# Kernel tuning notes

Measured on AMD Instinct MI355X. Metric: run time of the kernel, lower is better.

The kernel has to match this reference:

```python
import jax, jax.numpy as jnp
import numpy as np

B, D, H, E, C, TOPK = 16384, 2048, 2048, 6, 1024, 3

def setup_inputs() -> dict:
    key = jax.random.key(0)
    ks = jax.random.split(key, 8)
    s_d = 1.0 / np.sqrt(D)
    s_h = 1.0 / np.sqrt(H)
    return {
        "x": jax.random.normal(ks[0], (B, D), dtype=jnp.float32),
        "gate_W": jax.random.uniform(ks[1], (E, D), jnp.float32, -s_d, s_d),
        "gate_b": jax.random.uniform(ks[2], (E,), jnp.float32, -s_d, s_d),
        "W1": jax.random.uniform(ks[3], (E, H, D), jnp.float32, -s_d, s_d),
        "b1": jax.random.uniform(ks[4], (E, H), jnp.float32, -s_d, s_d),
        "W2": jax.random.uniform(ks[5], (E, C, H), jnp.float32, -s_h, s_h),
        "b2": jax.random.uniform(ks[6], (E, C), jnp.float32, -s_h, s_h),
    }

def reference(x, gate_W, gate_b, W1, b1, W2, b2):
    # gating: top-k sparse softmax
    gate_logits = x @ gate_W.T + gate_b                      # [B, E]
    topk_vals, topk_idx = jax.lax.top_k(gate_logits, TOPK)   # [B, K]
    neg_inf = jnp.finfo(gate_logits.dtype).min
    sparse = jnp.full_like(gate_logits, neg_inf)
    rows = jnp.arange(gate_logits.shape[0])[:, None]
    sparse = sparse.at[rows, topk_idx].set(topk_vals)
    gw = jax.nn.softmax(sparse, axis=-1)                     # [B, E]
    # dense experts: Linear -> GELU (exact, erf) -> Linear (dropout is eval no-op)
    h = jnp.einsum('bd,ehd->beh', x, W1) + b1[None]          # [B, E, H]
    h = jax.nn.gelu(h, approximate=False)
    expert_outs = jnp.einsum('beh,ech->bec', h, W2) + b2[None]  # [B, E, C]
    out = jnp.einsum('be,bec->bc', gw, expert_outs)          # masked combine
    return (out, gw)
```

## Files before the change

kernel.cpp:

```cpp
#include <hip/hip_runtime.h>
#include <hip/hip_bf16.h>
#include <math.h>

#define B_ 16384
#define D_ 2048
#define H_ 2048
#define E_ 6
#define C_ 1024

#define HALF_ (128 * 64)

typedef __attribute__((ext_vector_type(8))) short short8;
typedef __attribute__((ext_vector_type(4))) float f32x4;

__device__ __forceinline__ unsigned short f2bf(float f) {
    __hip_bfloat16 h = __float2bfloat16(f);
    return *reinterpret_cast<unsigned short*>(&h);
}

__device__ __forceinline__ void async_copy16(const unsigned short* g, unsigned short* l) {
    __builtin_amdgcn_global_load_lds(
        (const __attribute__((address_space(1))) unsigned int*)(g),
        (__attribute__((address_space(3))) unsigned int*)(l), 16, 0, 0);
}

__global__ void gate_kernel(const float* __restrict__ x, const float* __restrict__ gW,
                            const float* __restrict__ gb, float* __restrict__ gw_out,
                            int* __restrict__ counts, int* __restrict__ rowlist,
                            float* __restrict__ wtslist, unsigned short* __restrict__ xb) {
    int wave = threadIdx.x >> 6;
    int lane = threadIdx.x & 63;
    int row  = blockIdx.x * 4 + wave;
    const float* xr = x + (size_t)row * D_;
    unsigned short* xbr = xb + (size_t)row * D_;
    double acc[E_] = {0, 0, 0, 0, 0, 0};
    for (int i = 0; i < D_ / 64; ++i) {
        int d = i * 64 + lane;
        float xf = xr[d];
        xbr[d] = f2bf(xf);
        double xv = (double)xf;
#pragma unroll
        for (int e = 0; e < E_; ++e) acc[e] += xv * (double)gW[e * D_ + d];
    }
#pragma unroll
    for (int off = 32; off > 0; off >>= 1) {
#pragma unroll
        for (int e = 0; e < E_; ++e) acc[e] += __shfl_down(acc[e], off);
    }
    if (lane == 0) {
        double lg[E_];
#pragma unroll
        for (int e = 0; e < E_; ++e) lg[e] = acc[e] + (double)gb[e];
        bool used[E_] = {false, false, false, false, false, false};
        int idx[3]; double val[3];
        for (int k = 0; k < 3; ++k) {
            int best = -1; double bv = -1e300;
            for (int e = 0; e < E_; ++e)
                if (!used[e] && lg[e] > bv) { bv = lg[e]; best = e; }
            used[best] = true; idx[k] = best; val[k] = bv;
        }
        double m = val[0];
        double w[3]; double s = 0.0;
        for (int k = 0; k < 3; ++k) { w[k] = exp(val[k] - m); s += w[k]; }
        float gwv[E_] = {0.f, 0.f, 0.f, 0.f, 0.f, 0.f};
        for (int k = 0; k < 3; ++k) gwv[idx[k]] = (float)(w[k] / s);
#pragma unroll
        for (int e = 0; e < E_; ++e) gw_out[(size_t)row * E_ + e] = gwv[e];
        for (int k = 0; k < 3; ++k) {
            int e = idx[k];
            int pos = atomicAdd(&counts[e], 1);
            rowlist[(size_t)e * B_ + pos] = row * 3 + k;
            wtslist[(size_t)e * B_ + pos] = (float)(w[k] / s);
        }
    }
}

__global__ void cast_f32_bf16(const float* __restrict__ in, unsigned short* __restrict__ out, int n4) {
    int i = blockIdx.x * blockDim.x + threadIdx.x;
    if (i < n4) {
        float4 v = ((const float4*)in)[i];
        ushort4 u;
        u.x = f2bf(v.x); u.y = f2bf(v.y); u.z = f2bf(v.z); u.w = f2bf(v.w);
        ((ushort4*)out)[i] = u;
    }
}


#define PHASE_IN()                                                               \
    __builtin_amdgcn_sched_barrier(0);                                           \
    __builtin_amdgcn_s_barrier();                                                \
    asm volatile("s_waitcnt lgkmcnt(0)" ::: "memory");                           \
    __builtin_amdgcn_sched_barrier(0);                                           \
    __builtin_amdgcn_s_setprio(1);

#define PHASE_OUT()                                                              \
    __builtin_amdgcn_s_setprio(0);                                               \
    __builtin_amdgcn_sched_barrier(0);                                           \
    __builtin_amdgcn_s_barrier();

#define STAGE_A(dstbuf, koff)                                                    \
    _Pragma("unroll")                                                            \
    for (int h_ = 0; h_ < 2; ++h_)                                               \
        _Pragma("unroll")                                                        \
        for (int j_ = 0; j_ < 2; ++j_)                                           \
            async_copy16(asrc[h_][j_] + (koff),                                  \
                         (dstbuf) + h_ * HALF_ + (j_ * 512 + tid) * 8);

#define STAGE_B(dstbuf, koff)                                                    \
    _Pragma("unroll")                                                            \
    for (int h_ = 0; h_ < 2; ++h_)                                               \
        _Pragma("unroll")                                                        \
        for (int j_ = 0; j_ < 2; ++j_)                                           \
            async_copy16(bsrc[h_][j_] + (koff),                                  \
                         (dstbuf) + h_ * HALF_ + (j_ * 512 + tid) * 8);

#define MFMA_BF16 __builtin_amdgcn_mfma_f32_16x16x32_bf16

#define GEMM_CORE(KDIM)                                                          \
    int lane = tid & 63;                                                         \
    int wv = tid >> 6;                                                           \
    int wr = wv >> 2;                                        \
    int wc = wv & 3;                                         \
    int fm = lane & 15;                                                          \
    int kg = lane >> 4;                                                          \
    unsigned g0 = (unsigned)((kg ^ (fm & 7)) * 8);                               \
    unsigned g1 = (unsigned)(((4 + kg) ^ (fm & 7)) * 8);                         \
    unsigned aRB = (unsigned)(wr * HALF_ + fm * 64);                             \
    unsigned bRB = (unsigned)((wc >> 1) * HALF_ + ((wc & 1) * 64 + fm) * 64);    \
    f32x4 acc[8][4] = {};                                                        \
    const int NT = (KDIM) / 64;                                                  \
    STAGE_A(As, 0) STAGE_B(Bs, 0)                                                \
    STAGE_A(As + 2 * HALF_, 64) STAGE_B(Bs + 2 * HALF_, 64)                      \
    asm volatile("s_waitcnt vmcnt(8)" ::: "memory");                             \
    __builtin_amdgcn_s_barrier();                                                \
    __builtin_amdgcn_sched_barrier(0);                                           \
    for (int t = 0; t < NT; ++t) {                                               \
        unsigned short* Ab = As + (t & 1) * (2 * HALF_);                         \
        unsigned short* Bb = Bs + (t & 1) * (2 * HALF_);                         \
        const bool st = (t + 2 < NT);                                            \
        const int koff = (t + 2) * 64;                                           \
        const unsigned short* Ar0 = Ab + aRB + g0;                               \
        const unsigned short* Ar1 = Ab + aRB + g1;                               \
        const unsigned short* Br0 = Bb + bRB + g0;                               \
        const unsigned short* Br1 = Bb + bRB + g1;                               \
        short8 aF[4][2], bQ[2][2], bR[2][2];                                     \
                       \
        _Pragma("unroll")                                                        \
        for (int m = 0; m < 4; ++m) {                                            \
            aF[m][0] = *(const short8*)(Ar0 + m * 1024);                         \
            aF[m][1] = *(const short8*)(Ar1 + m * 1024);                         \
        }                                                                        \
        _Pragma("unroll")                                                        \
        for (int n = 0; n < 2; ++n) {                                            \
            bQ[n][0] = *(const short8*)(Br0 + n * 1024);                         \
            bQ[n][1] = *(const short8*)(Br1 + n * 1024);                         \
        }                                                                        \
        PHASE_IN()                                                               \
        _Pragma("unroll")                                                        \
        for (int m = 0; m < 4; ++m)                                              \
            _Pragma("unroll")                                                    \
            for (int n = 0; n < 2; ++n) {                                        \
                acc[m][n] = MFMA_BF16(aF[m][0], bQ[n][0], acc[m][n], 0, 0, 0);   \
                acc[m][n] = MFMA_BF16(aF[m][1], bQ[n][1], acc[m][n], 0, 0, 0);   \
            }                                                                    \
        PHASE_OUT()                                                              \
                                 \
        _Pragma("unroll")                                                        \
        for (int n = 0; n < 2; ++n) {                                            \
            bR[n][0] = *(const short8*)(Br0 + (2 + n) * 1024);                   \
            bR[n][1] = *(const short8*)(Br1 + (2 + n) * 1024);                   \
        }                                                                        \
        PHASE_IN()                                                               \
        _Pragma("unroll")                                                        \
        for (int m = 0; m < 4; ++m)                                              \
            _Pragma("unroll")                                                    \
            for (int n = 0; n < 2; ++n) {                                        \
                acc[m][2 + n] = MFMA_BF16(aF[m][0], bR[n][0], acc[m][2 + n], 0, 0, 0); \
                acc[m][2 + n] = MFMA_BF16(aF[m][1], bR[n][1], acc[m][2 + n], 0, 0, 0); \
            }                                                                    \
        PHASE_OUT()                                                               \
                   \
        _Pragma("unroll")                                                        \
        for (int m = 0; m < 4; ++m) {                                            \
            aF[m][0] = *(const short8*)(Ar0 + (4 + m) * 1024);                   \
            aF[m][1] = *(const short8*)(Ar1 + (4 + m) * 1024);                   \
        }                                                                        \
        if (st) { STAGE_B(Bb, koff) }                                            \
        PHASE_IN()                                                               \
        _Pragma("unroll")                                                        \
        for (int m = 0; m < 4; ++m)                                              \
            _Pragma("unroll")                                                    \
            for (int n = 0; n < 2; ++n) {                                        \
                acc[4 + m][n] = MFMA_BF16(aF[m][0], bQ[n][0], acc[4 + m][n], 0, 0, 0); \
                acc[4 + m][n] = MFMA_BF16(aF[m][1], bQ[n][1], acc[4 + m][n], 0, 0, 0); \
            }                                                                    \
        PHASE_OUT()                                                              \
                 \
        if (st) { STAGE_A(Ab, koff) }                                            \
        PHASE_IN()                                                               \
        _Pragma("unroll")                                                        \
        for (int m = 0; m < 4; ++m)                                              \
            _Pragma("unroll")                                                    \
            for (int n = 0; n < 2; ++n) {                                        \
                acc[4 + m][2 + n] = MFMA_BF16(aF[m][0], bR[n][0], acc[4 + m][2 + n], 0, 0, 0); \
                acc[4 + m][2 + n] = MFMA_BF16(aF[m][1], bR[n][1], acc[4 + m][2 + n], 0, 0, 0); \
            }                                                                    \
        __builtin_amdgcn_s_setprio(0);                                           \
        __builtin_amdgcn_sched_barrier(0);                                       \
        if (st) asm volatile("s_waitcnt vmcnt(8)" ::: "memory");                 \
        else    asm volatile("s_waitcnt vmcnt(0)" ::: "memory");                 \
        __builtin_amdgcn_s_barrier();                                            \
        __builtin_amdgcn_sched_barrier(0);                                       \
    }

__global__ __launch_bounds__(512, 2) void gemm1_kernel(
    const unsigned short* __restrict__ xb, const unsigned short* __restrict__ W1b,
    const float* __restrict__ b1, const int* __restrict__ counts,
    const int* __restrict__ rowlist, unsigned short* __restrict__ hbuf) {
    int e = blockIdx.z;
    int cnt = counts[e];
    int flat = blockIdx.x;
    int p  = (flat & 7) + ((flat >> 6) << 3);
    int nb = (flat >> 3) & 7;
    int m0 = p * 256;
    if (m0 >= cnt) return;
    int n0 = nb * 256;

    __shared__ __align__(16) unsigned short As[4 * HALF_];
    __shared__ __align__(16) unsigned short Bs[4 * HALF_];
    int tid = threadIdx.x;
    const int* rlist = rowlist + (size_t)e * B_;

    int rb = tid >> 3;
    int gth = ((tid & 7) ^ (rb & 7)) * 8;
    const unsigned short* asrc[2][2];
    const unsigned short* bsrc[2][2];
#pragma unroll
    for (int h = 0; h < 2; ++h)
#pragma unroll
        for (int j = 0; j < 2; ++j) {
            int r = h * 128 + j * 64 + rb;
            int idx = m0 + r; if (idx >= cnt) idx = cnt - 1;
            asrc[h][j] = xb + (size_t)(rlist[idx] / 3) * D_ + gth;
            bsrc[h][j] = W1b + (size_t)e * H_ * D_ + (size_t)(n0 + r) * D_ + gth;
        }

    GEMM_CORE(D_)

    int rlim = cnt - m0;
#pragma unroll
    for (int m = 0; m < 8; ++m) {
#pragma unroll
        for (int i = 0; i < 4; ++i) {
            int r = wr * 128 + m * 16 + kg * 4 + i;
            if (r < rlim) {
                size_t base = (size_t)rlist[m0 + r] * H_ + n0;
#pragma unroll
                for (int n = 0; n < 4; ++n) {
                    int col = wc * 64 + n * 16 + fm;
                    float v = acc[m][n][i] + b1[e * H_ + n0 + col];
                    v = 0.5f * v * (1.0f + erff(v * 0.70710678118654752f));
                    hbuf[base + col] = f2bf(v);
                }
            }
        }
    }
}

__global__ __launch_bounds__(512, 2) void gemm2_kernel(
    const unsigned short* __restrict__ hbuf, const unsigned short* __restrict__ W2b,
    const float* __restrict__ b2, const int* __restrict__ counts,
    const int* __restrict__ rowlist, const float* __restrict__ wtslist,
    float* __restrict__ sbuf, float* __restrict__ out) {
    int e = blockIdx.z;
    int cnt = counts[e];
    int flat = blockIdx.x;
    int p  = (flat & 7) + ((flat >> 5) << 3);
    int nb = (flat >> 3) & 3;
    int m0 = p * 256;
    if (m0 >= cnt) return;
    int n0 = nb * 256;

    __shared__ __align__(16) unsigned short As[4 * HALF_];
    __shared__ __align__(16) unsigned short Bs[4 * HALF_];
    int tid = threadIdx.x;
    const int* rlist = rowlist + (size_t)e * B_;
    const float* wlist = wtslist + (size_t)e * B_;

    int rb = tid >> 3;
    int gth = ((tid & 7) ^ (rb & 7)) * 8;
    const unsigned short* asrc[2][2];
    const unsigned short* bsrc[2][2];
#pragma unroll
    for (int h = 0; h < 2; ++h)
#pragma unroll
        for (int j = 0; j < 2; ++j) {
            int r = h * 128 + j * 64 + rb;
            int idx = m0 + r; if (idx >= cnt) idx = cnt - 1;
            asrc[h][j] = hbuf + (size_t)rlist[idx] * H_ + gth;
            bsrc[h][j] = W2b + (size_t)e * C_ * H_ + (size_t)(n0 + r) * H_ + gth;
        }

    GEMM_CORE(H_)

    int rlim = cnt - m0;
#pragma unroll
    for (int m = 0; m < 8; ++m) {
#pragma unroll
        for (int i = 0; i < 4; ++i) {
            int r = wr * 128 + m * 16 + kg * 4 + i;
            if (r < rlim) {
                int slot = rlist[m0 + r];
                float w  = wlist[m0 + r];
                if (sbuf) {
                    float* srow = sbuf + (size_t)slot * C_ + n0;
#pragma unroll
                    for (int n = 0; n < 4; ++n) {
                        int col = wc * 64 + n * 16 + fm;
                        srow[col] = (acc[m][n][i] + b2[e * C_ + n0 + col]) * w;
                    }
                } else {
                    float* orow = out + (size_t)(slot / 3) * C_ + n0;
#pragma unroll
                    for (int n = 0; n < 4; ++n) {
                        int col = wc * 64 + n * 16 + fm;
                        atomicAdd(&orow[col], (acc[m][n][i] + b2[e * C_ + n0 + col]) * w);
                    }
                }
            }
        }
    }
}

__global__ void combine_kernel(const float* __restrict__ sbuf, float* __restrict__ out) {
    int i   = blockIdx.x * 256 + threadIdx.x;
    int row = i >> 8;
    int c4  = i & 255;
    const float4* s4 = (const float4*)sbuf;
    size_t b = (size_t)row * 3 * 256 + c4;
    float4 a = s4[b], d = s4[b + 256], g = s4[b + 512];
    float4 r;
    r.x = a.x + d.x + g.x; r.y = a.y + d.y + g.y;
    r.z = a.z + d.z + g.z; r.w = a.w + d.w + g.w;
    ((float4*)out)[i] = r;
}

extern "C" void kernel_launch(void* const* d_in, const int* in_sizes, int n_in,
                              void* d_out, int out_size, void* d_ws, size_t ws_size,
                              hipStream_t stream) {
    const float* x  = (const float*)d_in[0];
    const float* gW = (const float*)d_in[1];
    const float* gb = (const float*)d_in[2];
    const float* W1 = (const float*)d_in[3];
    const float* b1 = (const float*)d_in[4];
    const float* W2 = (const float*)d_in[5];
    const float* b2 = (const float*)d_in[6];
    float* out    = (float*)d_out;
    float* gw_out = out + (size_t)B_ * C_;

    char* ws = (char*)d_ws;
    size_t off = 0;
    auto alloc = [&](size_t bytes) -> char* {
        char* p = ws + off;
        off = (off + bytes + 255) & ~(size_t)255;
        return p;
    };
    int*            counts  = (int*)alloc(E_ * 4);
    int*            rowlist = (int*)alloc((size_t)E_ * B_ * 4);
    float*          wtslist = (float*)alloc((size_t)E_ * B_ * 4);
    unsigned short* W2b     = (unsigned short*)alloc((size_t)E_ * C_ * H_ * 2);
    unsigned short* hbuf    = (unsigned short*)alloc((size_t)3 * B_ * H_ * 2);
    size_t region_off = off;
    unsigned short* xb      = (unsigned short*)alloc((size_t)B_ * D_ * 2);
    unsigned short* W1b     = (unsigned short*)alloc((size_t)E_ * H_ * D_ * 2);
    float*          sbuf    = (float*)(ws + region_off);
    size_t sbuf_end = region_off + (size_t)3 * B_ * C_ * 4;
    bool use_sbuf = (ws_size == 0) || (sbuf_end <= ws_size);
    (void)in_sizes; (void)n_in; (void)out_size;

    hipMemsetAsync(counts, 0, E_ * 4, stream);
    if (!use_sbuf) hipMemsetAsync(out, 0, (size_t)B_ * C_ * 4, stream);

    gate_kernel<<<B_ / 4, 256, 0, stream>>>(x, gW, gb, gw_out, counts, rowlist, wtslist, xb);
    cast_f32_bf16<<<(E_ * H_ * D_ / 4) / 256, 256, 0, stream>>>(W1, W1b, E_ * H_ * D_ / 4);
    cast_f32_bf16<<<(E_ * C_ * H_ / 4) / 256, 256, 0, stream>>>(W2, W2b, E_ * C_ * H_ / 4);
    gemm1_kernel<<<dim3(8 * (B_ / 256), 1, E_), 512, 0, stream>>>(xb, W1b, b1, counts, rowlist, hbuf);
    gemm2_kernel<<<dim3(4 * (B_ / 256), 1, E_), 512, 0, stream>>>(hbuf, W2b, b2, counts, rowlist, wtslist,
                                                                  use_sbuf ? sbuf : (float*)nullptr, out);
    if (use_sbuf)
        combine_kernel<<<(B_ * C_ / 4) / 256, 256, 0, stream>>>(sbuf, out);
}
```

Measured before the change: 1.873 ms.

## Trim GEMM barriers, compact hbuf per expert, add nontemporal stores

Rewrites the barrier structure of the shared GEMM main loop so that some phases rely only on an lgkmcnt wait and setprio, with no workgroup barrier, and moves the B-tile staging ahead of the A-fragment reads. The intermediate hidden buffer is now indexed by a per-expert prefix offset instead of the scattered slot index, so gemm2 reads contiguous rows. Stores to hbuf and sbuf, and the loads and stores in combine, become nontemporal to reduce cache pollution. Dropping barriers while async copies overwrite LDS buffers risks races if the remaining fences are not enough.

```diff
diff --git a/kernel.cpp b/kernel.cpp
--- a/kernel.cpp
+++ b/kernel.cpp
@@ -86,18 +86,6 @@
 }
 
 
-#define PHASE_IN()                                                               \
-    __builtin_amdgcn_sched_barrier(0);                                           \
-    __builtin_amdgcn_s_barrier();                                                \
-    asm volatile("s_waitcnt lgkmcnt(0)" ::: "memory");                           \
-    __builtin_amdgcn_sched_barrier(0);                                           \
-    __builtin_amdgcn_s_setprio(1);
-
-#define PHASE_OUT()                                                              \
-    __builtin_amdgcn_s_setprio(0);                                               \
-    __builtin_amdgcn_sched_barrier(0);                                           \
-    __builtin_amdgcn_s_barrier();
-
 #define STAGE_A(dstbuf, koff)                                                    \
     _Pragma("unroll")                                                            \
     for (int h_ = 0; h_ < 2; ++h_)                                               \
@@ -115,6 +103,14 @@
                          (dstbuf) + h_ * HALF_ + (j_ * 512 + tid) * 8);
 
 #define MFMA_BF16 __builtin_amdgcn_mfma_f32_16x16x32_bf16
+
+#define LGKM0_FENCE()                                                            \
+    asm volatile("s_waitcnt lgkmcnt(0)" ::: "memory");                           \
+    __builtin_amdgcn_sched_barrier(0);
+
+#define BARRIER_FENCE()                                                          \
+    __builtin_amdgcn_s_barrier();                                                \
+    __builtin_amdgcn_sched_barrier(0);
 
 #define GEMM_CORE(KDIM)                                                          \
     int lane = tid & 63;                                                         \
@@ -132,8 +128,7 @@
     STAGE_A(As, 0) STAGE_B(Bs, 0)                                                \
     STAGE_A(As + 2 * HALF_, 64) STAGE_B(Bs + 2 * HALF_, 64)                      \
     asm volatile("s_waitcnt vmcnt(8)" ::: "memory");                             \
-    __builtin_amdgcn_s_barrier();                                                \
-    __builtin_amdgcn_sched_barrier(0);                                           \
+    BARRIER_FENCE()                                                              \
     for (int t = 0; t < NT; ++t) {                                               \
         unsigned short* Ab = As + (t & 1) * (2 * HALF_);                         \
         unsigned short* Bb = Bs + (t & 1) * (2 * HALF_);                         \
@@ -144,7 +139,7 @@
         const unsigned short* Br0 = Bb + bRB + g0;                               \
         const unsigned short* Br1 = Bb + bRB + g1;                               \
         short8 aF[4][2], bQ[2][2], bR[2][2];                                     \
-                       \
+             \
         _Pragma("unroll")                                                        \
         for (int m = 0; m < 4; ++m) {                                            \
             aF[m][0] = *(const short8*)(Ar0 + m * 1024);                         \
@@ -155,7 +150,8 @@
             bQ[n][0] = *(const short8*)(Br0 + n * 1024);                         \
             bQ[n][1] = *(const short8*)(Br1 + n * 1024);                         \
         }                                                                        \
-        PHASE_IN()                                                               \
+        LGKM0_FENCE()                                                            \
+        __builtin_amdgcn_s_setprio(1);                                           \
         _Pragma("unroll")                                                        \
         for (int m = 0; m < 4; ++m)                                              \
             _Pragma("unroll")                                                    \
@@ -163,14 +159,16 @@
                 acc[m][n] = MFMA_BF16(aF[m][0], bQ[n][0], acc[m][n], 0, 0, 0);   \
                 acc[m][n] = MFMA_BF16(aF[m][1], bQ[n][1], acc[m][n], 0, 0, 0);   \
             }                                                                    \
-        PHASE_OUT()                                                              \
-                                 \
+        __builtin_amdgcn_s_setprio(0);                                           \
+               \
         _Pragma("unroll")                                                        \
         for (int n = 0; n < 2; ++n) {                                            \
             bR[n][0] = *(const short8*)(Br0 + (2 + n) * 1024);                   \
             bR[n][1] = *(const short8*)(Br1 + (2 + n) * 1024);                   \
         }                                                                        \
-        PHASE_IN()                                                               \
+        LGKM0_FENCE()                                                            \
+        BARRIER_FENCE()                                                          \
+        __builtin_amdgcn_s_setprio(1);                                           \
         _Pragma("unroll")                                                        \
         for (int m = 0; m < 4; ++m)                                              \
             _Pragma("unroll")                                                    \
@@ -178,15 +176,17 @@
                 acc[m][2 + n] = MFMA_BF16(aF[m][0], bR[n][0], acc[m][2 + n], 0, 0, 0); \
                 acc[m][2 + n] = MFMA_BF16(aF[m][1], bR[n][1], acc[m][2 + n], 0, 0, 0); \
             }                                                                    \
-        PHASE_OUT()                                                               \
-                   \
+        __builtin_amdgcn_s_setprio(0);                                           \
+         \
+        if (st) { STAGE_B(Bb, koff) }                                            \
         _Pragma("unroll")                                                        \
         for (int m = 0; m < 4; ++m) {                                            \
             aF[m][0] = *(const short8*)(Ar0 + (4 + m) * 1024);                   \
             aF[m][1] = *(const short8*)(Ar1 + (4 + m) * 1024);                   \
         }                                                                        \
-        if (st) { STAGE_B(Bb, koff) }                                            \
-        PHASE_IN()                                                               \
+        LGKM0_FENCE()                                                            \
+        BARRIER_FENCE()                                                          \
+        __builtin_amdgcn_s_setprio(1);                                           \
         _Pragma("unroll")                                                        \
         for (int m = 0; m < 4; ++m)                                              \
             _Pragma("unroll")                                                    \
@@ -194,10 +194,10 @@
                 acc[4 + m][n] = MFMA_BF16(aF[m][0], bQ[n][0], acc[4 + m][n], 0, 0, 0); \
                 acc[4 + m][n] = MFMA_BF16(aF[m][1], bQ[n][1], acc[4 + m][n], 0, 0, 0); \
             }                                                                    \
-        PHASE_OUT()                                                              \
-                 \
+        __builtin_amdgcn_s_setprio(0);                                           \
+         \
         if (st) { STAGE_A(Ab, koff) }                                            \
-        PHASE_IN()                                                               \
+        __builtin_amdgcn_s_setprio(1);                                           \
         _Pragma("unroll")                                                        \
         for (int m = 0; m < 4; ++m)                                              \
             _Pragma("unroll")                                                    \
@@ -209,8 +209,8 @@
         __builtin_amdgcn_sched_barrier(0);                                       \
         if (st) asm volatile("s_waitcnt vmcnt(8)" ::: "memory");                 \
         else    asm volatile("s_waitcnt vmcnt(0)" ::: "memory");                 \
-        __builtin_amdgcn_s_barrier();                                            \
         __builtin_amdgcn_sched_barrier(0);                                       \
+        BARRIER_FENCE()                                                          \
     }
 
 __global__ __launch_bounds__(512, 2) void gemm1_kernel(
@@ -219,6 +219,9 @@
     const int* __restrict__ rowlist, unsigned short* __restrict__ hbuf) {
     int e = blockIdx.z;
     int cnt = counts[e];
+    int eoff = 0;
+#pragma unroll
+    for (int i = 0; i < E_; ++i) if (i < e) eoff += counts[i];
     int flat = blockIdx.x;
     int p  = (flat & 7) + ((flat >> 6) << 3);
     int nb = (flat >> 3) & 7;
@@ -254,13 +257,13 @@
         for (int i = 0; i < 4; ++i) {
             int r = wr * 128 + m * 16 + kg * 4 + i;
             if (r < rlim) {
-                size_t base = (size_t)rlist[m0 + r] * H_ + n0;
+                size_t base = (size_t)(eoff + m0 + r) * H_ + n0;
 #pragma unroll
                 for (int n = 0; n < 4; ++n) {
                     int col = wc * 64 + n * 16 + fm;
                     float v = acc[m][n][i] + b1[e * H_ + n0 + col];
                     v = 0.5f * v * (1.0f + erff(v * 0.70710678118654752f));
-                    hbuf[base + col] = f2bf(v);
+                    __builtin_nontemporal_store(f2bf(v), &hbuf[base + col]);
                 }
             }
         }
@@ -274,6 +277,9 @@
     float* __restrict__ sbuf, float* __restrict__ out) {
     int e = blockIdx.z;
     int cnt = counts[e];
+    int eoff = 0;
+#pragma unroll
+    for (int i = 0; i < E_; ++i) if (i < e) eoff += counts[i];
     int flat = blockIdx.x;
     int p  = (flat & 7) + ((flat >> 5) << 3);
     int nb = (flat >> 3) & 3;
@@ -297,7 +303,7 @@
         for (int j = 0; j < 2; ++j) {
             int r = h * 128 + j * 64 + rb;
             int idx = m0 + r; if (idx >= cnt) idx = cnt - 1;
-            asrc[h][j] = hbuf + (size_t)rlist[idx] * H_ + gth;
+            asrc[h][j] = hbuf + (size_t)(eoff + idx) * H_ + gth;
             bsrc[h][j] = W2b + (size_t)e * C_ * H_ + (size_t)(n0 + r) * H_ + gth;
         }
 
@@ -317,7 +323,8 @@
 #pragma unroll
                     for (int n = 0; n < 4; ++n) {
                         int col = wc * 64 + n * 16 + fm;
-                        srow[col] = (acc[m][n][i] + b2[e * C_ + n0 + col]) * w;
+                        __builtin_nontemporal_store(
+                            (acc[m][n][i] + b2[e * C_ + n0 + col]) * w, &srow[col]);
                     }
                 } else {
                     float* orow = out + (size_t)(slot / 3) * C_ + n0;
@@ -336,13 +343,13 @@
     int i   = blockIdx.x * 256 + threadIdx.x;
     int row = i >> 8;
     int c4  = i & 255;
-    const float4* s4 = (const float4*)sbuf;
+    const f32x4* s4 = (const f32x4*)sbuf;
     size_t b = (size_t)row * 3 * 256 + c4;
-    float4 a = s4[b], d = s4[b + 256], g = s4[b + 512];
-    float4 r;
-    r.x = a.x + d.x + g.x; r.y = a.y + d.y + g.y;
-    r.z = a.z + d.z + g.z; r.w = a.w + d.w + g.w;
-    ((float4*)out)[i] = r;
+    f32x4 a = __builtin_nontemporal_load(&s4[b]);
+    f32x4 d = __builtin_nontemporal_load(&s4[b + 256]);
+    f32x4 g = __builtin_nontemporal_load(&s4[b + 512]);
+    f32x4 r = a + d + g;
+    __builtin_nontemporal_store(r, &((f32x4*)out)[i]);
 }
 
 extern "C" void kernel_launch(void* const* d_in, const int* in_sizes, int n_in,
```

Result: faster. 1.764 ms (-5.8%).
